# Kernel optimization log

Measured on AMD Instinct MI355X. Metric: run time of the kernel, lower is better.

Reference implementation:

```python
import jax, jax.numpy as jnp
import numpy as np

B, L, LOCAL_DIM, M = 4096, 256, 2, 64

def setup_inputs() -> dict:
    key = jax.random.key(0)
    k1, k2 = jax.random.split(key)
    samples = jax.random.randint(k1, (B, L), 0, LOCAL_DIM, dtype=jnp.int32)
    # epsilon near 1 so the product over L=256 sites is numerically stable
    epsilon = 1.0 + 0.05 * jax.random.normal(k2, (LOCAL_DIM, M, L), dtype=jnp.float32)
    return {"samples": samples, "epsilon": epsilon}

def reference(samples, epsilon):
    # samples: (B, L) int occupancies in [0, local_dim)
    # epsilon: (local_dim, M, L)
    # qGPS full path with no_syms: out[b] = sum_m prod_l epsilon[samples[b,l], m, l]
    Ls = samples.shape[-1]
    eps_t = jnp.transpose(epsilon, (2, 0, 1))          # (L, local_dim, M)
    gathered = eps_t[jnp.arange(Ls)[None, :], samples]  # (B, L, M) gather by occupancy
    site_prod = jnp.prod(gathered, axis=1)              # (B, M) product over sites
    return jnp.sum(site_prod, axis=-1)                  # (B,) sum over support dim M
```

## Files before the change

kernel.cpp:

```cpp
#include <hip/hip_runtime.h>

#define BQ 4096
#define LQ 256
#define MQ 64

__global__ __launch_bounds__(256) void qgps_pack(const int* __restrict__ samples,
                                                 unsigned long long* __restrict__ packed) {
    const int wave = threadIdx.x >> 6;
    const int lane = threadIdx.x & 63;
    const int b = blockIdx.x * 4 + wave;
    const int* row = samples + b * LQ;
#pragma unroll
    for (int c2 = 0; c2 < 4; ++c2) {
        int s = row[c2 * 64 + lane];
        unsigned long long mask = __ballot(s & 1);
        if (lane == 0) packed[c2 * BQ + b] = mask;
    }
}

__global__ __launch_bounds__(64) void qgps_prep(const float* __restrict__ eps,
                                                float* __restrict__ rm1,
                                                float* __restrict__ C) {
    const int m = blockIdx.x;
    const int lane = threadIdx.x;
    const float* e0 = eps + m * LQ;
    const float* e1 = eps + (MQ + m) * LQ;
    float q = 1.0f;
#pragma unroll
    for (int k = 0; k < 4; ++k) {
        int l = lane * 4 + k;
        float a = e0[l];
        q *= a;
        rm1[m * LQ + l] = e1[l] / a - 1.0f;
    }
#pragma unroll
    for (int off = 32; off > 0; off >>= 1)
        q *= __shfl_xor(q, off, 64);
    if (lane == 0) C[m] = q;
}

__global__ __launch_bounds__(256) void qgps_main(const unsigned long long* __restrict__ packed,
                                                 const float* __restrict__ rm1,
                                                 const float* __restrict__ C,
                                                 float* __restrict__ out) {
    __shared__ float red[4][64];
    const int wave = __builtin_amdgcn_readfirstlane(threadIdx.x >> 6);
    const int lane = threadIdx.x & 63;
    const int bg = blockIdx.x >> 4;
    const int mb = blockIdx.x & 15;
    const int m  = mb * 4 + wave;
    const int b  = bg * 64 + lane;

    const float* __restrict__ rrow = rm1 + m * LQ;

    float p0 = 1.0f, p1 = 1.0f;
    for (int c2 = 0; c2 < 4; ++c2) {
        unsigned long long w = packed[c2 * BQ + b];
        unsigned int wlo = (unsigned int)w, whi = (unsigned int)(w >> 32);
        const float* r0 = rrow + c2 * 64;
#pragma unroll
        for (int j = 0; j < 32; j += 2) {
            float f0 = (float)((wlo >> j) & 1u);
            float f1 = (float)((wlo >> (j + 1)) & 1u);
            p0 *= 1.0f + f0 * r0[j];
            p1 *= 1.0f + f1 * r0[j + 1];
        }
        const float* r1 = r0 + 32;
#pragma unroll
        for (int j = 0; j < 32; j += 2) {
            float f0 = (float)((whi >> j) & 1u);
            float f1 = (float)((whi >> (j + 1)) & 1u);
            p0 *= 1.0f + f0 * r1[j];
            p1 *= 1.0f + f1 * r1[j + 1];
        }
    }
    red[wave][lane] = C[m] * (p0 * p1);
    __syncthreads();
    if (wave == 0) {
        float s = (red[0][lane] + red[1][lane]) + (red[2][lane] + red[3][lane]);
        atomicAdd(&out[b], s);
    }
}

extern "C" void kernel_launch(void* const* d_in, const int* in_sizes, int n_in,
                              void* d_out, int out_size, void* d_ws, size_t ws_size,
                              hipStream_t stream) {
    const int* samples = (const int*)d_in[0];
    const float* eps = (const float*)d_in[1];
    float* out = (float*)d_out;

    unsigned long long* packed = (unsigned long long*)d_ws;
    float* rm1 = (float*)((char*)d_ws + 4 * BQ * sizeof(unsigned long long));
    float* C   = rm1 + MQ * LQ;

    hipMemsetAsync(out, 0, BQ * sizeof(float), stream);

    qgps_pack<<<BQ / 4, 256, 0, stream>>>(samples, packed);
    qgps_prep<<<MQ, 64, 0, stream>>>(eps, rm1, C);
    qgps_main<<<1024, 256, 0, stream>>>(packed, rm1, C, out);
}
```

Measured before the change: 67.98 us.

## Fuse pack, prep and output zeroing into one launch; stage rm1 in LDS with bitmask FMA

The memset and the two preprocessing kernels are folded into a single launch whose block ranges do bit-packing, epsilon ratio prep, and zeroing of the output. This cuts launch count from four to two. The main kernel now stages its rm1 slice in shared memory and reads it as float4. Each factor is computed as an FMA with the ratio masked by a bitfield-extract sign mask, replacing the int-to-float conversion and multiply. The cost is an extra barrier and LDS traffic per block.

```diff
diff --git a/kernel.cpp b/kernel.cpp
--- a/kernel.cpp
+++ b/kernel.cpp
@@ -4,74 +4,89 @@
 #define LQ 256
 #define MQ 64
 
-__global__ __launch_bounds__(256) void qgps_pack(const int* __restrict__ samples,
-                                                 unsigned long long* __restrict__ packed) {
+__global__ __launch_bounds__(256) void qgps_prep_all(const int* __restrict__ samples,
+                                                     const float* __restrict__ eps,
+                                                     unsigned long long* __restrict__ packed,
+                                                     float* __restrict__ rm1,
+                                                     float* __restrict__ C,
+                                                     float* __restrict__ out) {
+    const int blk = blockIdx.x;
     const int wave = threadIdx.x >> 6;
     const int lane = threadIdx.x & 63;
-    const int b = blockIdx.x * 4 + wave;
-    const int* row = samples + b * LQ;
+    if (blk < 1024) {
+        const int b = blk * 4 + wave;
+        const int* row = samples + b * LQ;
 #pragma unroll
-    for (int c2 = 0; c2 < 4; ++c2) {
-        int s = row[c2 * 64 + lane];
-        unsigned long long mask = __ballot(s & 1);
-        if (lane == 0) packed[c2 * BQ + b] = mask;
+        for (int c2 = 0; c2 < 4; ++c2) {
+            unsigned long long mask = __ballot(row[c2 * 64 + lane] & 1);
+            if (lane == 0) packed[c2 * BQ + b] = mask;
+        }
+    } else if (blk < 1040) {
+        const int m = (blk - 1024) * 4 + wave;
+        const float* e0 = eps + m * LQ;
+        const float* e1 = eps + (MQ + m) * LQ;
+        float q = 1.0f;
+#pragma unroll
+        for (int k = 0; k < 4; ++k) {
+            int l = lane * 4 + k;
+            float a = e0[l];
+            q *= a;
+            rm1[m * LQ + l] = e1[l] / a - 1.0f;
+        }
+#pragma unroll
+        for (int off = 32; off > 0; off >>= 1) q *= __shfl_xor(q, off, 64);
+        if (lane == 0) C[m] = q;
+    } else {
+        float4* o4 = (float4*)out;
+        o4[(blk - 1040) * 256 + threadIdx.x] = make_float4(0.f, 0.f, 0.f, 0.f);
     }
 }
 
-__global__ __launch_bounds__(64) void qgps_prep(const float* __restrict__ eps,
-                                                float* __restrict__ rm1,
-                                                float* __restrict__ C) {
-    const int m = blockIdx.x;
-    const int lane = threadIdx.x;
-    const float* e0 = eps + m * LQ;
-    const float* e1 = eps + (MQ + m) * LQ;
-    float q = 1.0f;
-#pragma unroll
-    for (int k = 0; k < 4; ++k) {
-        int l = lane * 4 + k;
-        float a = e0[l];
-        q *= a;
-        rm1[m * LQ + l] = e1[l] / a - 1.0f;
-    }
-#pragma unroll
-    for (int off = 32; off > 0; off >>= 1)
-        q *= __shfl_xor(q, off, 64);
-    if (lane == 0) C[m] = q;
+__device__ __forceinline__ float bit_and_r(unsigned w, int j, float r) {
+    int msk = __builtin_amdgcn_sbfe((int)w, j, 1);
+    return __uint_as_float(__float_as_uint(r) & (unsigned)msk);
 }
 
 __global__ __launch_bounds__(256) void qgps_main(const unsigned long long* __restrict__ packed,
                                                  const float* __restrict__ rm1,
                                                  const float* __restrict__ C,
                                                  float* __restrict__ out) {
+    __shared__ float lr[1024];
     __shared__ float red[4][64];
-    const int wave = __builtin_amdgcn_readfirstlane(threadIdx.x >> 6);
-    const int lane = threadIdx.x & 63;
+    const int tid = threadIdx.x;
+    const int wave = tid >> 6;
+    const int lane = tid & 63;
     const int bg = blockIdx.x >> 4;
     const int mb = blockIdx.x & 15;
-    const int m  = mb * 4 + wave;
-    const int b  = bg * 64 + lane;
 
-    const float* __restrict__ rrow = rm1 + m * LQ;
+#pragma unroll
+    for (int i = 0; i < 4; ++i) lr[tid + i * 256] = rm1[mb * 1024 + tid + i * 256];
+    __syncthreads();
+
+    const int b = bg * 64 + lane;
+    const int m = mb * 4 + wave;
+    const float4* r4 = (const float4*)&lr[wave * 256];
 
     float p0 = 1.0f, p1 = 1.0f;
+#pragma unroll
     for (int c2 = 0; c2 < 4; ++c2) {
         unsigned long long w = packed[c2 * BQ + b];
         unsigned int wlo = (unsigned int)w, whi = (unsigned int)(w >> 32);
-        const float* r0 = rrow + c2 * 64;
 #pragma unroll
-        for (int j = 0; j < 32; j += 2) {
-            float f0 = (float)((wlo >> j) & 1u);
-            float f1 = (float)((wlo >> (j + 1)) & 1u);
-            p0 *= 1.0f + f0 * r0[j];
-            p1 *= 1.0f + f1 * r0[j + 1];
+        for (int q = 0; q < 8; ++q) {
+            float4 r = r4[c2 * 16 + q];
+            p0 = fmaf(p0, bit_and_r(wlo, 4 * q + 0, r.x), p0);
+            p1 = fmaf(p1, bit_and_r(wlo, 4 * q + 1, r.y), p1);
+            p0 = fmaf(p0, bit_and_r(wlo, 4 * q + 2, r.z), p0);
+            p1 = fmaf(p1, bit_and_r(wlo, 4 * q + 3, r.w), p1);
         }
-        const float* r1 = r0 + 32;
 #pragma unroll
-        for (int j = 0; j < 32; j += 2) {
-            float f0 = (float)((whi >> j) & 1u);
-            float f1 = (float)((whi >> (j + 1)) & 1u);
-            p0 *= 1.0f + f0 * r1[j];
-            p1 *= 1.0f + f1 * r1[j + 1];
+        for (int q = 0; q < 8; ++q) {
+            float4 r = r4[c2 * 16 + 8 + q];
+            p0 = fmaf(p0, bit_and_r(whi, 4 * q + 0, r.x), p0);
+            p1 = fmaf(p1, bit_and_r(whi, 4 * q + 1, r.y), p1);
+            p0 = fmaf(p0, bit_and_r(whi, 4 * q + 2, r.z), p0);
+            p1 = fmaf(p1, bit_and_r(whi, 4 * q + 3, r.w), p1);
         }
     }
     red[wave][lane] = C[m] * (p0 * p1);
@@ -91,11 +106,8 @@
 
     unsigned long long* packed = (unsigned long long*)d_ws;
     float* rm1 = (float*)((char*)d_ws + 4 * BQ * sizeof(unsigned long long));
-    float* C   = rm1 + MQ * LQ;
+    float* C = rm1 + MQ * LQ;
 
-    hipMemsetAsync(out, 0, BQ * sizeof(float), stream);
-
-    qgps_pack<<<BQ / 4, 256, 0, stream>>>(samples, packed);
-    qgps_prep<<<MQ, 64, 0, stream>>>(eps, rm1, C);
+    qgps_prep_all<<<1044, 256, 0, stream>>>(samples, eps, packed, rm1, C, out);
     qgps_main<<<1024, 256, 0, stream>>>(packed, rm1, C, out);
 }
```

After: 64.36 us. 1.06x faster.
